# Kernel tuning notes

Measured on AMD Instinct MI355X. Metric: run time of the kernel, lower is better.

## Reference

```python
import jax, jax.numpy as jnp
import numpy as np
import itertools

DIM = 384
KEY_DIM = 32
NUM_HEADS = 8
ATTN_RATIO = 4
RESOLUTION = 7
D = ATTN_RATIO * KEY_DIM          # 128
DH = D * NUM_HEADS                # 1024
H_QKV = DH + 2 * KEY_DIM * NUM_HEADS  # 1536
B = 2048
N = RESOLUTION ** 2               # 49


def _build_bias_idxs():
    points = list(itertools.product(range(RESOLUTION), range(RESOLUTION)))
    attention_offsets = {}
    idxs = []
    for p1 in points:
        for p2 in points:
            offset = (abs(p1[0] - p2[0]), abs(p1[1] - p2[1]))
            if offset not in attention_offsets:
                attention_offsets[offset] = len(attention_offsets)
            idxs.append(attention_offsets[offset])
    return np.array(idxs, dtype=np.int32).reshape(N, N), len(attention_offsets)


def setup_inputs() -> dict:
    key = jax.random.key(0)
    ks = jax.random.split(key, 6)
    bias_idxs_np, n_offsets = _build_bias_idxs()  # n_offsets == 49 for resolution 7
    x = jax.random.normal(ks[0], (B, N, DIM), dtype=jnp.float32)
    qkv_w = jax.random.normal(ks[1], (H_QKV, DIM), dtype=jnp.float32) * (DIM ** -0.5)
    qkv_b = jnp.zeros((H_QKV,), dtype=jnp.float32)
    proj_w = jax.random.normal(ks[2], (DIM, DH), dtype=jnp.float32) * (DH ** -0.5)
    proj_b = jnp.zeros((DIM,), dtype=jnp.float32)
    attn_bias = jax.random.normal(ks[3], (NUM_HEADS, n_offsets), dtype=jnp.float32) * 0.02
    bias_idxs = jnp.asarray(bias_idxs_np)
    return {"x": x, "qkv_w": qkv_w, "qkv_b": qkv_b, "proj_w": proj_w,
            "proj_b": proj_b, "attn_bias": attn_bias, "bias_idxs": bias_idxs}


def reference(x, qkv_w, qkv_b, proj_w, proj_b, attn_bias, bias_idxs):
    Bb, Nn, _ = x.shape
    scale = KEY_DIM ** -0.5
    qkv = x @ qkv_w.T + qkv_b                       # [B, N, 1536]
    qkv = qkv.reshape(Bb, Nn, NUM_HEADS, KEY_DIM + KEY_DIM + D)
    q = qkv[..., :KEY_DIM]                          # [B, N, H, kd]
    k = qkv[..., KEY_DIM:2 * KEY_DIM]               # [B, N, H, kd]
    v = qkv[..., 2 * KEY_DIM:]                      # [B, N, H, d]
    bias = attn_bias[:, bias_idxs]                  # [H, N, N] gathered rel-pos bias
    attn = jnp.einsum('bnhk,bmhk->bhnm', q, k) * scale + bias
    attn = jax.nn.softmax(attn, axis=-1)
    out = jnp.einsum('bhnm,bmhd->bnhd', attn, v).reshape(Bb, Nn, DH)
    return out @ proj_w.T + proj_b                  # [B, N, dim]
```

## Files before the change

### kernel.cpp

```cpp
#include <hip/hip_runtime.h>
#include <cstddef>
#include <cstdint>

#define TOK    49
#define KD     32
#define NH     8
#define DHEAD  128
#define HQKV   1536
#define DHTOT  1024
#define DIMM   384

typedef unsigned short u16;
typedef float  f32x4  __attribute__((ext_vector_type(4)));
typedef __bf16 bf16x8 __attribute__((ext_vector_type(8)));

typedef const __attribute__((address_space(1))) void gas_void;
typedef __attribute__((address_space(3))) void las_void;

static __device__ __forceinline__ u16 f2bf(float f) {
    unsigned int u = __builtin_bit_cast(unsigned int, f);
    return (u16)((u + 0x7fffu + ((u >> 16) & 1u)) >> 16);
}

static __device__ __forceinline__ int swz(int row, int c) {
    return (row << 6) + ((((c >> 3) ^ (row & 7)) << 3) | (c & 7));
}

static __device__ __forceinline__ int swzV(int row, int c) {
    return (row << 6) + ((((c >> 3) ^ (row & 7) ^ ((row >> 3) & 7)) << 3) | (c & 7));
}

static __device__ __forceinline__ int xcd_chunk(int bid, int nwg) {
    const int xcd = bid & 7, slot = bid >> 3;
    const int q = nwg >> 3, r = nwg & 7;
    return (xcd < r ? xcd * (q + 1) : r * (q + 1) + (xcd - r) * q) + slot;
}

#define BAR() __builtin_amdgcn_s_barrier()
#define WAIT_VM8() asm volatile("s_waitcnt vmcnt(8)" ::: "memory")
#define WAIT_VM0() asm volatile("s_waitcnt vmcnt(0)" ::: "memory")
#define LGKM0_BAR() do { asm volatile("s_waitcnt lgkmcnt(0)" ::: "memory"); \
                         __builtin_amdgcn_s_barrier(); } while (0)

__global__ __launch_bounds__(256)
void cast_swz(const float* __restrict__ in, u16* __restrict__ out, int K8, long nchunk)
{
    long i = (long)blockIdx.x * 256 + threadIdx.x;
    const long stride = (long)gridDim.x * 256;
    for (; i < nchunk; i += stride) {
        const long row = i / K8;
        const int  c8  = (int)(i - row * K8);
        const int  slot = c8 & 7, tpan = c8 >> 3;
        float4 v0 = reinterpret_cast<const float4*>(in)[i * 2];
        float4 v1 = reinterpret_cast<const float4*>(in)[i * 2 + 1];
        uint4 o;
        o.x = f2bf(v0.x) | ((unsigned)f2bf(v0.y) << 16);
        o.y = f2bf(v0.z) | ((unsigned)f2bf(v0.w) << 16);
        o.z = f2bf(v1.x) | ((unsigned)f2bf(v1.y) << 16);
        o.w = f2bf(v1.z) | ((unsigned)f2bf(v1.w) << 16);
        *reinterpret_cast<uint4*>(out + row * (long)K8 * 8 + tpan * 64 +
                                  ((slot ^ ((int)row & 7)) << 3)) = o;
    }
}

__global__ __launch_bounds__(256)
void bias_expand(const float* __restrict__ attn_bias, const int* __restrict__ idxs,
                 float* __restrict__ bias_full, int n_off)
{
    int i = blockIdx.x * 256 + threadIdx.x;
    if (i < NH * TOK * TOK) {
        int h = i / (TOK * TOK), s = i - h * (TOK * TOK);
        bias_full[i] = attn_bias[h * n_off + idxs[s]];
    }
}

static __device__ __forceinline__ int frag_off(int row, int ks8fg) {
    return (row << 6) + (((ks8fg ^ (row & 7)) << 3));
}

__global__ __launch_bounds__(256)
void gemm_qkv(const u16* __restrict__ A,
              const u16* __restrict__ W,
              const float* __restrict__ bias,
              u16* __restrict__ qkvb, int M)
{
    const int K = DIMM;
    const int NB = HQKV / 128;
    const int nwg = (M / 128) * NB;
    const int wgid = xcd_chunk(blockIdx.x, nwg);
    const int bm = (wgid / NB) * 128;
    const int bn = (wgid % NB) * 128;

    __shared__ u16 Alds[2][128 * 64];
    __shared__ u16 Blds[2][128 * 64];

    const int t    = threadIdx.x;
    const int lane = t & 63;
    const int wv   = t >> 6;
    const int wr   = wv >> 1;
    const int wc   = wv & 1;

    const int lrow = lane >> 3;
    const int lcol = (lane & 7) * 8;
    const int frow = lane & 15;
    const int fg   = lane >> 4;

    f32x4 acc[4][4];
    #pragma unroll
    for (int mi = 0; mi < 4; ++mi)
        #pragma unroll
        for (int ni = 0; ni < 4; ++ni) acc[mi][ni] = (f32x4)0.0f;

    auto STAGE = [&](int buf, int k0) {
        #pragma unroll
        for (int i = 0; i < 4; ++i) {
            const int c   = i * 4 + wv;
            const int row = c * 8 + lrow;
            __builtin_amdgcn_global_load_lds((gas_void*)(A + (size_t)(bm + row) * K + k0 + lcol),
                                             (las_void*)(&Alds[buf][c * 512]), 16, 0, 0);
            __builtin_amdgcn_global_load_lds((gas_void*)(W + (size_t)(bn + row) * K + k0 + lcol),
                                             (las_void*)(&Blds[buf][c * 512]), 16, 0, 0);
        }
    };

    STAGE(0, 0);
    STAGE(1, 64);

    const int NT = 6;
    for (int ts = 0; ts < NT; ++ts) {
        if (ts < NT - 1) { WAIT_VM8(); }
        else             { WAIT_VM0(); }
        BAR();
        const u16* Ab = Alds[ts & 1];
        const u16* Bb = Blds[ts & 1];
        #pragma unroll
        for (int ks = 0; ks < 2; ++ks) {
            const int sl = ks * 4 + fg;
            bf16x8 af[4], bf[4];
            #pragma unroll
            for (int mi = 0; mi < 4; ++mi)
                af[mi] = *reinterpret_cast<const bf16x8*>(&Ab[frag_off(wr * 64 + mi * 16 + frow, sl)]);
            #pragma unroll
            for (int ni = 0; ni < 4; ++ni)
                bf[ni] = *reinterpret_cast<const bf16x8*>(&Bb[frag_off(wc * 64 + ni * 16 + frow, sl)]);
            #pragma unroll
            for (int mi = 0; mi < 4; ++mi)
                #pragma unroll
                for (int ni = 0; ni < 4; ++ni)
                    acc[mi][ni] = __builtin_amdgcn_mfma_f32_16x16x32_bf16(af[mi], bf[ni], acc[mi][ni], 0, 0, 0);
        }
        BAR();
        if (ts < NT - 2) STAGE(ts & 1, (ts + 2) * 64);
    }

    const int rbase = (lane >> 4) * 4;
    #pragma unroll
    for (int ni = 0; ni < 4; ++ni) {
        const int col = bn + wc * 64 + ni * 16 + frow;
        const float bv = bias[col];
        #pragma unroll
        for (int mi = 0; mi < 4; ++mi) {
            #pragma unroll
            for (int j = 0; j < 4; ++j) {
                const int row = bm + wr * 64 + mi * 16 + rbase + j;
                qkvb[(size_t)row * HQKV + col] = f2bf(acc[mi][ni][j] + bv);
            }
        }
    }
}

__global__ __launch_bounds__(256)
void gemm_bf16_nt(const u16* __restrict__ A, const u16* __restrict__ W,
                  const float* __restrict__ bias, float* __restrict__ C,
                  int M, int N, int K)
{
    const int NB = N / 128;
    const int nwg = (M / 128) * NB;
    const int wgid = xcd_chunk(blockIdx.x, nwg);
    const int bm = (wgid / NB) * 128;
    const int bn = (wgid % NB) * 128;

    __shared__ u16 Alds[2][128 * 64];
    __shared__ u16 Blds[2][128 * 64];

    const int t    = threadIdx.x;
    const int lane = t & 63;
    const int wv   = t >> 6;
    const int wr   = wv >> 1;
    const int wc   = wv & 1;

    const int lrow = lane >> 3;
    const int lcol = (lane & 7) * 8;
    const int frow = lane & 15;
    const int fg   = lane >> 4;

    f32x4 acc[4][4];
    #pragma unroll
    for (int mi = 0; mi < 4; ++mi)
        #pragma unroll
        for (int ni = 0; ni < 4; ++ni) acc[mi][ni] = (f32x4)0.0f;

    auto STAGE = [&](int buf, int k0) {
        #pragma unroll
        for (int i = 0; i < 4; ++i) {
            const int c   = i * 4 + wv;
            const int row = c * 8 + lrow;
            __builtin_amdgcn_global_load_lds((gas_void*)(A + (size_t)(bm + row) * K + k0 + lcol),
                                             (las_void*)(&Alds[buf][c * 512]), 16, 0, 0);
            __builtin_amdgcn_global_load_lds((gas_void*)(W + (size_t)(bn + row) * K + k0 + lcol),
                                             (las_void*)(&Blds[buf][c * 512]), 16, 0, 0);
        }
    };

    const int NT = K / 64;
    STAGE(0, 0);
    STAGE(1, 64);

    for (int ts = 0; ts < NT; ++ts) {
        if (ts < NT - 1) { WAIT_VM8(); }
        else             { WAIT_VM0(); }
        BAR();
        const u16* Ab = Alds[ts & 1];
        const u16* Bb = Blds[ts & 1];
        #pragma unroll
        for (int ks = 0; ks < 2; ++ks) {
            const int sl = ks * 4 + fg;
            bf16x8 af[4], bf[4];
            #pragma unroll
            for (int mi = 0; mi < 4; ++mi)
                af[mi] = *reinterpret_cast<const bf16x8*>(&Ab[frag_off(wr * 64 + mi * 16 + frow, sl)]);
            #pragma unroll
            for (int ni = 0; ni < 4; ++ni)
                bf[ni] = *reinterpret_cast<const bf16x8*>(&Bb[frag_off(wc * 64 + ni * 16 + frow, sl)]);
            #pragma unroll
            for (int mi = 0; mi < 4; ++mi)
                #pragma unroll
                for (int ni = 0; ni < 4; ++ni)
                    acc[mi][ni] = __builtin_amdgcn_mfma_f32_16x16x32_bf16(af[mi], bf[ni], acc[mi][ni], 0, 0, 0);
        }
        BAR();
        if (ts < NT - 2) STAGE(ts & 1, (ts + 2) * 64);
    }

    const int rbase = (lane >> 4) * 4;
    #pragma unroll
    for (int ni = 0; ni < 4; ++ni) {
        const int col = bn + wc * 64 + ni * 16 + frow;
        const float bv = bias[col];
        #pragma unroll
        for (int mi = 0; mi < 4; ++mi) {
            #pragma unroll
            for (int j = 0; j < 4; ++j) {
                const int row = bm + wr * 64 + mi * 16 + rbase + j;
                C[(size_t)row * N + col] = acc[mi][ni][j] + bv;
            }
        }
    }
}

#define NCH 5

struct Regs { uint4 v[NCH]; };

static __device__ __forceinline__ void load_regs(Regs& r, const u16* __restrict__ base, int t)
{
    #pragma unroll
    for (int k = 0; k < NCH; ++k) {
        const int idx = t + k * 256;
        if (idx < TOK * 24) {
            const int n = idx / 24, c = idx - n * 24;
            r.v[k] = *reinterpret_cast<const uint4*>(base + (size_t)n * HQKV + c * 8);
        }
    }
}

static __device__ __forceinline__ void write_lds(const Regs& r, u16* __restrict__ QK,
                                                 u16* __restrict__ V, int t)
{
    #pragma unroll
    for (int k = 0; k < NCH; ++k) {
        const int idx = t + k * 256;
        if (idx < TOK * 24) {
            const int n = idx / 24, c24 = idx - n * 24;
            if (c24 < 8) {
                *reinterpret_cast<uint4*>(&QK[(n << 6) + ((c24 ^ (n & 7)) << 3)]) = r.v[k];
            } else {
                const int d0 = (c24 - 8) * 8;
                u16 vals[8];
                *reinterpret_cast<uint4*>(vals) = r.v[k];
                #pragma unroll
                for (int e = 0; e < 8; ++e)
                    V[swzV(d0 + e, n)] = vals[e];
            }
        }
    }
}

static __device__ __forceinline__ void attn_head(
    const u16* __restrict__ QK, const u16* __restrict__ V,
    float* __restrict__ S, u16* __restrict__ Ps,
    const float* __restrict__ bh_bias, u16* __restrict__ ab,
    int b, int h, int t)
{
    const int lane = t & 63;
    const int w    = t >> 6;
    const int fr   = lane & 15;
    const int fg   = lane >> 4;

    bf16x8 qf = *reinterpret_cast<const bf16x8*>(&QK[swz(16 * w + fr, fg * 8)]);
    f32x4 sacc[4];
    #pragma unroll
    for (int nj = 0; nj < 4; ++nj) {
        bf16x8 kf = *reinterpret_cast<const bf16x8*>(&QK[swz(16 * nj + fr, 32 + fg * 8)]);
        sacc[nj] = __builtin_amdgcn_mfma_f32_16x16x32_bf16(qf, kf, (f32x4)0.0f, 0, 0, 0);
    }

    const float scale = 0.17677669529663687f;
    #pragma unroll
    for (int nj = 0; nj < 4; ++nj) {
        #pragma unroll
        for (int j = 0; j < 4; ++j) {
            const int row = 16 * w + fg * 4 + j;
            const int col = 16 * nj + fr;
            const int rn = row < TOK ? row : TOK - 1;
            const int cm = col < TOK ? col : TOK - 1;
            S[row * 80 + col] = sacc[nj][j] * scale + bh_bias[rn * TOK + cm];
        }
    }
    LGKM0_BAR();

    {
        const int n = t >> 2, j = t & 3;
        const float* Sr = &S[n * 80];
        float v[16];
        #pragma unroll
        for (int e = 0; e < 8; ++e) v[e]     = Sr[8 * j + e];
        #pragma unroll
        for (int e = 0; e < 8; ++e) v[8 + e] = Sr[32 + 8 * j + e];

        float mx = -1e30f;
        #pragma unroll
        for (int e = 0; e < 8; ++e) mx = fmaxf(mx, v[e]);
        #pragma unroll
        for (int e = 0; e < 8; ++e)
            if (32 + 8 * j + e < TOK) mx = fmaxf(mx, v[8 + e]);
        mx = fmaxf(mx, __shfl_xor(mx, 1, 4));
        mx = fmaxf(mx, __shfl_xor(mx, 2, 4));

        float sum = 0.f;
        #pragma unroll
        for (int e = 0; e < 8; ++e) { v[e] = __expf(v[e] - mx); sum += v[e]; }
        #pragma unroll
        for (int e = 0; e < 8; ++e) {
            const float ev = (32 + 8 * j + e < TOK) ? __expf(v[8 + e] - mx) : 0.f;
            v[8 + e] = ev; sum += ev;
        }
        sum += __shfl_xor(sum, 1, 4);
        sum += __shfl_xor(sum, 2, 4);
        const float inv = 1.f / sum;

        uint4 o;
        o.x = f2bf(v[0] * inv)  | ((unsigned)f2bf(v[1] * inv)  << 16);
        o.y = f2bf(v[2] * inv)  | ((unsigned)f2bf(v[3] * inv)  << 16);
        o.z = f2bf(v[4] * inv)  | ((unsigned)f2bf(v[5] * inv)  << 16);
        o.w = f2bf(v[6] * inv)  | ((unsigned)f2bf(v[7] * inv)  << 16);
        *reinterpret_cast<uint4*>(&Ps[swz(n, 8 * j)]) = o;
        o.x = f2bf(v[8] * inv)  | ((unsigned)f2bf(v[9] * inv)  << 16);
        o.y = f2bf(v[10] * inv) | ((unsigned)f2bf(v[11] * inv) << 16);
        o.z = f2bf(v[12] * inv) | ((unsigned)f2bf(v[13] * inv) << 16);
        o.w = f2bf(v[14] * inv) | ((unsigned)f2bf(v[15] * inv) << 16);
        *reinterpret_cast<uint4*>(&Ps[swz(n, 32 + 8 * j)]) = o;
    }
    LGKM0_BAR();

    f32x4 oacc[8];
    #pragma unroll
    for (int nj = 0; nj < 8; ++nj) oacc[nj] = (f32x4)0.0f;
    #pragma unroll
    for (int ks = 0; ks < 2; ++ks) {
        bf16x8 pf = *reinterpret_cast<const bf16x8*>(&Ps[swz(16 * w + fr, ks * 32 + fg * 8)]);
        #pragma unroll
        for (int nj = 0; nj < 8; ++nj) {
            bf16x8 vf = *reinterpret_cast<const bf16x8*>(&V[swzV(16 * nj + fr, ks * 32 + fg * 8)]);
            oacc[nj] = __builtin_amdgcn_mfma_f32_16x16x32_bf16(pf, vf, oacc[nj], 0, 0, 0);
        }
    }

    #pragma unroll
    for (int nj = 0; nj < 8; ++nj) {
        const int d = 16 * nj + fr;
        const int c = h * DHEAD + d;
        const int tp = c >> 6, sl = (c >> 3) & 7, cc = c & 7;
        #pragma unroll
        for (int j = 0; j < 4; ++j) {
            const int n = 16 * w + fg * 4 + j;
            if (n < TOK) {
                const int gr = b * TOK + n;
                ab[(size_t)gr * DHTOT + (tp << 6) + (((sl ^ (gr & 7)) << 3) | cc)] = f2bf(oacc[nj][j]);
            }
        }
    }
}

__global__ __launch_bounds__(256)
void attn_mfma(const u16* __restrict__ qkvb,
               const float* __restrict__ bias_full,
               u16* __restrict__ ab)
{
    __shared__ __align__(16) u16  QKs[2][64 * 64];
    __shared__ __align__(16) u16  Vts[2][128 * 64];
    __shared__ __align__(16) float S[64 * 80];
    __shared__ __align__(16) u16  Ps[64 * 64];

    const int t = threadIdx.x;
    const int b = blockIdx.x;
    const u16* base = qkvb + (size_t)b * TOK * HQKV;

    Regs ra, rb;
    load_regs(ra, base + 0 * 192, t);

    for (int i = t; i < 128 * 2 * 2; i += 256) {
        const int bufi = i >> 9, r = (i >> 1) & 127, sl = 6 + (i & 1);
        *reinterpret_cast<uint4*>(&Vts[bufi][(r << 6) +
            (((sl ^ (r & 7) ^ ((r >> 3) & 7)) & 7) << 3)]) = make_uint4(0, 0, 0, 0);
    }
    LGKM0_BAR();

    #pragma unroll
    for (int hp = 0; hp < 4; ++hp) {
        const int h0 = hp * 2, h1 = hp * 2 + 1;

        write_lds(ra, QKs[0], Vts[0], t);
        load_regs(rb, base + h1 * 192, t);
        LGKM0_BAR();
        attn_head(QKs[0], Vts[0], S, Ps, bias_full + h0 * (TOK * TOK), ab, b, h0, t);

        write_lds(rb, QKs[1], Vts[1], t);
        if (hp < 3) load_regs(ra, base + (h0 + 2) * 192, t);
        LGKM0_BAR();
        attn_head(QKs[1], Vts[1], S, Ps, bias_full + h1 * (TOK * TOK), ab, b, h1, t);
    }
}

extern "C" void kernel_launch(void* const* d_in, const int* in_sizes, int n_in,
                              void* d_out, int out_size, void* d_ws, size_t ws_size,
                              hipStream_t stream)
{
    const float* x         = (const float*)d_in[0];
    const float* qkv_w     = (const float*)d_in[1];
    const float* qkv_b     = (const float*)d_in[2];
    const float* proj_w    = (const float*)d_in[3];
    const float* proj_b    = (const float*)d_in[4];
    const float* attn_bias = (const float*)d_in[5];
    const int*   bias_idxs = (const int*)d_in[6];

    const int Mtot  = in_sizes[0] / DIMM;
    const int Btot  = Mtot / TOK;
    const int n_off = in_sizes[5] / NH;

    const size_t nWq = (size_t)HQKV * DIMM;
    const size_t nWp = (size_t)DIMM * DHTOT;
    float* bias_full = (float*)d_ws;
    u16*   wq        = (u16*)((char*)d_ws + 76832);
    u16*   wp        = wq + nWq;
    u16*   dyn       = wp + nWp;
    const size_t fixed_bytes = 76832 + (nWq + nWp) * sizeof(u16);
    const size_t per_batch = (size_t)TOK * (DIMM + HQKV + DHTOT) * 2;

    if (ws_size <= fixed_bytes) return;
    long BcL = (long)((ws_size - fixed_bytes) / per_batch);
    int Bc = (int)((BcL / 128) * 128);
    if (Bc <= 0) return;
    if (Bc > Btot) Bc = Btot;

    cast_swz<<<dim3(288), 256, 0, stream>>>(qkv_w, wq, DIMM / 8, (long)HQKV * (DIMM / 8));
    cast_swz<<<dim3(192), 256, 0, stream>>>(proj_w, wp, DHTOT / 8, (long)DIMM * (DHTOT / 8));
    bias_expand<<<dim3((NH * TOK * TOK + 255) / 256), 256, 0, stream>>>(attn_bias, bias_idxs, bias_full, n_off);

    for (int b0 = 0; b0 < Btot; b0 += Bc) {
        const int bc = (b0 + Bc <= Btot) ? Bc : (Btot - b0);
        const int Mc = bc * TOK;

        u16* xb   = dyn;
        u16* qkvb = xb   + (size_t)Bc * TOK * DIMM;
        u16* abb  = qkvb + (size_t)Bc * TOK * HQKV;

        const float* xc   = x + (size_t)b0 * TOK * DIMM;
        float*       outc = (float*)d_out + (size_t)b0 * TOK * DIMM;

        cast_swz<<<dim3(2048), 256, 0, stream>>>(xc, xb, DIMM / 8, (long)Mc * (DIMM / 8));

        gemm_qkv<<<dim3((Mc / 128) * (HQKV / 128)), 256, 0, stream>>>(xb, wq, qkv_b, qkvb, Mc);

        attn_mfma<<<dim3(bc), 256, 0, stream>>>(qkvb, bias_full, abb);

        gemm_bf16_nt<<<dim3((Mc / 128) * (DIMM / 128)), 256, 0, stream>>>(abb, wp, proj_b, outc, Mc, DIMM, DHTOT);
    }
}
```

Measured before the change: 725.3 us.

## Split attention kernel across head pairs with a 2D grid and single LDS buffer

The attention kernel now launches one block per (batch, head-pair) instead of one block per batch handling all eight heads. This gives four times as many blocks, and halving the QK/V shared-memory buffers lowers LDS use per block, which should raise occupancy. The first head is loaded straight into LDS while the second head is prefetched into registers. The cost is less cross-head pipelining inside a block, plus a scalar per-element V transpose store for the first head.

```diff
diff --git a/kernel.cpp b/kernel.cpp
--- a/kernel.cpp
+++ b/kernel.cpp
@@ -259,7 +259,6 @@
 }
 
 #define NCH 5
-
 struct Regs { uint4 v[NCH]; };
 
 static __device__ __forceinline__ void load_regs(Regs& r, const u16* __restrict__ base, int t)
@@ -407,39 +406,52 @@
                const float* __restrict__ bias_full,
                u16* __restrict__ ab)
 {
-    __shared__ __align__(16) u16  QKs[2][64 * 64];
-    __shared__ __align__(16) u16  Vts[2][128 * 64];
+    __shared__ __align__(16) u16  QKs[64 * 64];
+    __shared__ __align__(16) u16  Vts[128 * 64];
     __shared__ __align__(16) float S[64 * 80];
     __shared__ __align__(16) u16  Ps[64 * 64];
 
-    const int t = threadIdx.x;
-    const int b = blockIdx.x;
+    const int t  = threadIdx.x;
+    const int b  = blockIdx.x;
+    const int h0 = blockIdx.y * 2;
+    const int h1 = h0 + 1;
     const u16* base = qkvb + (size_t)b * TOK * HQKV;
 
-    Regs ra, rb;
-    load_regs(ra, base + 0 * 192, t);
-
-    for (int i = t; i < 128 * 2 * 2; i += 256) {
-        const int bufi = i >> 9, r = (i >> 1) & 127, sl = 6 + (i & 1);
-        *reinterpret_cast<uint4*>(&Vts[bufi][(r << 6) +
-            (((sl ^ (r & 7) ^ ((r >> 3) & 7)) & 7) << 3)]) = make_uint4(0, 0, 0, 0);
-    }
+    if (t < 128 * 2) {
+        const int row = t >> 1, sl = 6 + (t & 1);
+        *reinterpret_cast<uint4*>(&Vts[(row << 6) +
+            (((sl ^ (row & 7) ^ ((row >> 3) & 7)) & 7) << 3)]) = make_uint4(0, 0, 0, 0);
+    }
+    __syncthreads();
+
+    const u16* qrow = base + h0 * 192;
+    for (int flat = t; flat < TOK * 24; flat += 256) {
+        const int n = flat / 24, c24 = flat - n * 24;
+        uint4 u = *reinterpret_cast<const uint4*>(qrow + (size_t)n * HQKV + c24 * 8);
+        if (c24 < 8) {
+            *reinterpret_cast<uint4*>(&QKs[(n << 6) + ((c24 ^ (n & 7)) << 3)]) = u;
+        } else {
+            const int d0 = (c24 - 8) * 8;
+            u16 vals[8];
+            *reinterpret_cast<uint4*>(vals) = u;
+            #pragma unroll
+            for (int e = 0; e < 8; ++e)
+                Vts[swzV(d0 + e, n)] = vals[e];
+        }
+    }
+
+    Regs rb;
+    load_regs(rb, base + h1 * 192, t);
+
     LGKM0_BAR();
 
-    #pragma unroll
-    for (int hp = 0; hp < 4; ++hp) {
-        const int h0 = hp * 2, h1 = hp * 2 + 1;
-
-        write_lds(ra, QKs[0], Vts[0], t);
-        load_regs(rb, base + h1 * 192, t);
-        LGKM0_BAR();
-        attn_head(QKs[0], Vts[0], S, Ps, bias_full + h0 * (TOK * TOK), ab, b, h0, t);
-
-        write_lds(rb, QKs[1], Vts[1], t);
-        if (hp < 3) load_regs(ra, base + (h0 + 2) * 192, t);
-        LGKM0_BAR();
-        attn_head(QKs[1], Vts[1], S, Ps, bias_full + h1 * (TOK * TOK), ab, b, h1, t);
-    }
+    attn_head(QKs, Vts, S, Ps, bias_full + h0 * (TOK * TOK), ab, b, h0, t);
+    LGKM0_BAR();
+
+    write_lds(rb, QKs, Vts, t);
+    LGKM0_BAR();
+
+    attn_head(QKs, Vts, S, Ps, bias_full + h1 * (TOK * TOK), ab, b, h1, t);
 }
 
 extern "C" void kernel_launch(void* const* d_in, const int* in_sizes, int n_in,
@@ -492,7 +504,7 @@
 
         gemm_qkv<<<dim3((Mc / 128) * (HQKV / 128)), 256, 0, stream>>>(xb, wq, qkv_b, qkvb, Mc);
 
-        attn_mfma<<<dim3(bc), 256, 0, stream>>>(qkvb, bias_full, abb);
+        attn_mfma<<<dim3(bc, NH / 2), 256, 0, stream>>>(qkvb, bias_full, abb);
 
         gemm_bf16_nt<<<dim3((Mc / 128) * (DIMM / 128)), 256, 0, stream>>>(abb, wp, proj_b, outc, Mc, DIMM, DHTOT);
     }
```

Result: faster. 664.3 us (-8.4%).
